# Kernel tuning notes

Measured on AMD Instinct MI355X. Metric: run time of the kernel, lower is better.

The kernel has to match this reference:

```python
import jax, jax.numpy as jnp
import numpy as np


def setup_inputs() -> dict:
    key = jax.random.key(0)
    ks = jax.random.split(key, 5)
    B, C, L, A = 32, 512, 8192, 128
    x = jax.random.normal(ks[0], (B, C, L), dtype=jnp.float32)
    Wq = jax.random.normal(ks[1], (A, C), dtype=jnp.float32) * 0.02
    Wk = jax.random.normal(ks[2], (A, C), dtype=jnp.float32) * 0.02
    Wv = jax.random.normal(ks[3], (A, C), dtype=jnp.float32) * 0.02
    Wout = jax.random.normal(ks[4], (C, A), dtype=jnp.float32) * 0.02
    return {"x": x, "Wq": Wq, "Wk": Wk, "Wv": Wv, "Wout": Wout, "center_idx": 4096}


def reference(x, Wq, Wk, Wv, Wout, center_idx):
    # x: [B, C, L]; W*: [attn_dim, C] (torch Linear weight layout); Wout: [C, attn_dim]
    A = Wq.shape[0]
    xc = x[:, :, center_idx]                      # [B, C] center feature
    q = xc @ Wq.T                                 # [B, A]
    xt = jnp.swapaxes(x, 1, 2)                    # [B, L, C]
    k = jnp.einsum('blc,ac->bla', xt, Wk)         # [B, L, A]
    v = jnp.einsum('blc,ac->bla', xt, Wv)         # [B, L, A]
    attn = jnp.einsum('bla,ba->bl', k, q) / jnp.sqrt(jnp.asarray(A, x.dtype))
    w = jax.nn.softmax(attn, axis=-1)             # [B, L]
    pooled = jnp.einsum('bla,bl->ba', v, w)       # [B, A]
    pooled = pooled @ Wout.T                      # [B, C]
    return (pooled, w)
```

## Files before the change

### kernel.cpp

```cpp
#include <hip/hip_runtime.h>
#include <math.h>

#define B_ 32
#define C_ 512
#define L_ 8192
#define A_ 128

__global__ __launch_bounds__(128) void k1_qk(const float* __restrict__ x,
                                             const float* __restrict__ Wq,
                                             const float* __restrict__ Wk,
                                             const int* __restrict__ cidx,
                                             float* __restrict__ qk) {
  __shared__ float xc[C_];
  __shared__ float q[A_];
  const int b = blockIdx.x, tid = threadIdx.x;
  const int ci = cidx[0];
  const float* xb = x + (size_t)b * C_ * L_;
  for (int c = tid; c < C_; c += 128) xc[c] = xb[(size_t)c * L_ + ci];
  __syncthreads();
  {
    float acc = 0.f;
    const float* wq = Wq + tid * C_;
    for (int c = 0; c < C_; ++c) acc += xc[c] * wq[c];
    q[tid] = acc;
  }
  __syncthreads();
  const float scale = 0.08838834764831845f;
  for (int c = tid; c < C_; c += 128) {
    float s = 0.f;
    for (int a = 0; a < A_; ++a) s += q[a] * Wk[a * C_ + c];
    qk[b * C_ + c] = s * scale;
  }
}

__global__ __launch_bounds__(128) void k2_attn(const float* __restrict__ x,
                                               const float* __restrict__ qk,
                                               float* __restrict__ attn) {
  __shared__ float qks[C_];
  const int b = blockIdx.y, tid = threadIdx.x;
  const int l = blockIdx.x * 512 + tid * 4;
  for (int c = tid; c < C_; c += 128) qks[c] = qk[b * C_ + c];
  __syncthreads();
  const float* xb = x + (size_t)b * C_ * L_ + l;
  float4 acc = make_float4(0.f, 0.f, 0.f, 0.f);
#pragma unroll 8
  for (int c = 0; c < C_; ++c) {
    const float4 xv4 = *reinterpret_cast<const float4*>(xb + (size_t)c * L_);
    const float s = qks[c];
    acc.x += s * xv4.x;
    acc.y += s * xv4.y;
    acc.z += s * xv4.z;
    acc.w += s * xv4.w;
  }
  *reinterpret_cast<float4*>(attn + b * L_ + l) = acc;
}

__global__ __launch_bounds__(256) void k3_softmax(const float* __restrict__ attn,
                                                  float* __restrict__ w) {
  const int b = blockIdx.x, tid = threadIdx.x;
  const float* ab = attn + b * L_;
  float4 vals[8];
  float m = -INFINITY;
#pragma unroll
  for (int i = 0; i < 8; ++i) {
    vals[i] = *reinterpret_cast<const float4*>(ab + (size_t)(i * 256 + tid) * 4);
    m = fmaxf(m, fmaxf(fmaxf(vals[i].x, vals[i].y), fmaxf(vals[i].z, vals[i].w)));
  }
  __shared__ float sm[256];
  sm[tid] = m;
  __syncthreads();
  for (int s = 128; s > 0; s >>= 1) {
    if (tid < s) sm[tid] = fmaxf(sm[tid], sm[tid + s]);
    __syncthreads();
  }
  m = sm[0];
  __syncthreads();
  float sum = 0.f;
#pragma unroll
  for (int i = 0; i < 8; ++i) {
    vals[i].x = __expf(vals[i].x - m);
    vals[i].y = __expf(vals[i].y - m);
    vals[i].z = __expf(vals[i].z - m);
    vals[i].w = __expf(vals[i].w - m);
    sum += vals[i].x + vals[i].y + vals[i].z + vals[i].w;
  }
  sm[tid] = sum;
  __syncthreads();
  for (int s = 128; s > 0; s >>= 1) {
    if (tid < s) sm[tid] += sm[tid + s];
    __syncthreads();
  }
  const float inv = 1.f / sm[0];
  float* wb = w + b * L_;
#pragma unroll
  for (int i = 0; i < 8; ++i) {
    float4 o;
    o.x = vals[i].x * inv;
    o.y = vals[i].y * inv;
    o.z = vals[i].z * inv;
    o.w = vals[i].w * inv;
    *reinterpret_cast<float4*>(wb + (size_t)(i * 256 + tid) * 4) = o;
  }
}

__global__ __launch_bounds__(256) void k4_xv(const float* __restrict__ x,
                                             const float* __restrict__ w,
                                             float* __restrict__ xv) {
  const int b = blockIdx.y, c = blockIdx.x, tid = threadIdx.x;
  const float* row = x + ((size_t)b * C_ + c) * L_;
  const float* wb = w + b * L_;
  float acc = 0.f;
#pragma unroll
  for (int i = 0; i < 8; ++i) {
    const int l = (i * 256 + tid) * 4;
    const float4 xr = *reinterpret_cast<const float4*>(row + l);
    const float4 wr = *reinterpret_cast<const float4*>(wb + l);
    acc += xr.x * wr.x + xr.y * wr.y + xr.z * wr.z + xr.w * wr.w;
  }
  __shared__ float sm[256];
  sm[tid] = acc;
  __syncthreads();
  for (int s = 128; s > 0; s >>= 1) {
    if (tid < s) sm[tid] += sm[tid + s];
    __syncthreads();
  }
  if (tid == 0) xv[b * C_ + c] = sm[0];
}

__global__ __launch_bounds__(128) void k5_out(const float* __restrict__ xv,
                                              const float* __restrict__ Wv,
                                              const float* __restrict__ Wout,
                                              float* __restrict__ out) {
  __shared__ float xvs[C_];
  __shared__ float pv[A_];
  const int b = blockIdx.x, tid = threadIdx.x;
  for (int c = tid; c < C_; c += 128) xvs[c] = xv[b * C_ + c];
  __syncthreads();
  {
    float acc = 0.f;
    const float* wv = Wv + tid * C_;
    for (int c = 0; c < C_; ++c) acc += xvs[c] * wv[c];
    pv[tid] = acc;
  }
  __syncthreads();
  for (int co = tid; co < C_; co += 128) {
    float acc = 0.f;
    const float* wo = Wout + co * A_;
    for (int a = 0; a < A_; ++a) acc += pv[a] * wo[a];
    out[b * C_ + co] = acc;
  }
}

extern "C" void kernel_launch(void* const* d_in, const int* in_sizes, int n_in,
                              void* d_out, int out_size, void* d_ws, size_t ws_size,
                              hipStream_t stream) {
  const float* x = (const float*)d_in[0];
  const float* Wq = (const float*)d_in[1];
  const float* Wk = (const float*)d_in[2];
  const float* Wv = (const float*)d_in[3];
  const float* Wout = (const float*)d_in[4];
  const int* cidx = (const int*)d_in[5];

  float* out_pooled = (float*)d_out;
  float* out_w = out_pooled + B_ * C_;

  float* qk = (float*)d_ws;
  float* attn = qk + B_ * C_;
  float* xv = attn + (size_t)B_ * L_;

  k1_qk<<<B_, 128, 0, stream>>>(x, Wq, Wk, cidx, qk);
  k2_attn<<<dim3(L_ / 512, B_), 128, 0, stream>>>(x, qk, attn);
  k3_softmax<<<B_, 256, 0, stream>>>(attn, out_w);
  k4_xv<<<dim3(C_, B_), 256, 0, stream>>>(x, out_w, xv);
  k5_out<<<B_, 128, 0, stream>>>(xv, Wv, Wout, out_pooled);
}
```

Baseline: 813.4 us.

## Fuse attention scores, local softmax and x·w pooling into one pass over x

Each block now loads a 512x32 tile of x into shared memory once. From that tile it computes the attention logits, a tile-local max and exp-sum, and partial weighted sums of x with the unnormalised probabilities. Small combine kernels then rescale the partials with the global max and normaliser, flash-attention style. This removes the second full read of the 537 MB x tensor. The cost is a larger workspace for per-tile partials (B*256*C floats), plus reading attn again to produce w.

Measured after the change: 790.1 us. 2.9% less time.

```diff
diff --git a/kernel.cpp b/kernel.cpp
--- a/kernel.cpp
+++ b/kernel.cpp
@@ -5,6 +5,8 @@
 #define C_ 512
 #define L_ 8192
 #define A_ 128
+#define LT_ 32
+#define NBLK_ (L_ / LT_)
 
 __global__ __launch_bounds__(128) void k1_qk(const float* __restrict__ x,
                                              const float* __restrict__ Wq,
@@ -33,98 +35,129 @@
   }
 }
 
-__global__ __launch_bounds__(128) void k2_attn(const float* __restrict__ x,
-                                               const float* __restrict__ qk,
-                                               float* __restrict__ attn) {
+__global__ __launch_bounds__(256) void kf_fused(const float* __restrict__ x,
+                                                const float* __restrict__ qk,
+                                                float* __restrict__ attn,
+                                                float* __restrict__ mpart,
+                                                float* __restrict__ zpart,
+                                                float* __restrict__ xvp) {
+  __shared__ float xs[C_][LT_ + 1];
   __shared__ float qks[C_];
-  const int b = blockIdx.y, tid = threadIdx.x;
-  const int l = blockIdx.x * 512 + tid * 4;
-  for (int c = tid; c < C_; c += 128) qks[c] = qk[b * C_ + c];
-  __syncthreads();
-  const float* xb = x + (size_t)b * C_ * L_ + l;
-  float4 acc = make_float4(0.f, 0.f, 0.f, 0.f);
+  __shared__ float p[LT_];
+  __shared__ float red[8][LT_];
+  const int tid = threadIdx.x;
+  const int blk = blockIdx.x;
+  const int b = blockIdx.y;
+  const int l0 = blk * LT_;
+  const float* xb = x + (size_t)b * C_ * L_;
+
+  qks[tid] = qk[b * C_ + tid];
+  qks[tid + 256] = qk[b * C_ + tid + 256];
+#pragma unroll
+  for (int i = 0; i < 16; ++i) {
+    const int idx = i * 256 + tid;
+    const int c = idx >> 3;
+    const int li = (idx & 7) * 4;
+    const float4 v = *reinterpret_cast<const float4*>(xb + (size_t)c * L_ + l0 + li);
+    xs[c][li] = v.x; xs[c][li + 1] = v.y; xs[c][li + 2] = v.z; xs[c][li + 3] = v.w;
+  }
+  __syncthreads();
+
+  const int l = tid & 31, g = tid >> 5;
+  {
+    float part = 0.f;
+    const int cbase = g * 64;
 #pragma unroll 8
-  for (int c = 0; c < C_; ++c) {
-    const float4 xv4 = *reinterpret_cast<const float4*>(xb + (size_t)c * L_);
-    const float s = qks[c];
-    acc.x += s * xv4.x;
-    acc.y += s * xv4.y;
-    acc.z += s * xv4.z;
-    acc.w += s * xv4.w;
-  }
-  *reinterpret_cast<float4*>(attn + b * L_ + l) = acc;
-}
-
-__global__ __launch_bounds__(256) void k3_softmax(const float* __restrict__ attn,
-                                                  float* __restrict__ w) {
+    for (int c = cbase; c < cbase + 64; ++c) part += qks[c] * xs[c][l];
+    red[g][l] = part;
+  }
+  __syncthreads();
+  if (tid < 32) {
+    float a = 0.f;
+#pragma unroll
+    for (int gg = 0; gg < 8; ++gg) a += red[gg][l];
+    attn[b * L_ + l0 + l] = a;
+    float m = a;
+#pragma unroll
+    for (int o = 16; o > 0; o >>= 1) m = fmaxf(m, __shfl_xor(m, o, 32));
+    const float pv = __expf(a - m);
+    float z = pv;
+#pragma unroll
+    for (int o = 16; o > 0; o >>= 1) z += __shfl_xor(z, o, 32);
+    p[l] = pv;
+    if (l == 0) { mpart[b * NBLK_ + blk] = m; zpart[b * NBLK_ + blk] = z; }
+  }
+  __syncthreads();
+
+#pragma unroll
+  for (int k = 0; k < 2; ++k) {
+    const int c = tid + k * 256;
+    float acc = 0.f;
+#pragma unroll
+    for (int ll = 0; ll < LT_; ++ll) acc += p[ll] * xs[c][ll];
+    xvp[((size_t)b * NBLK_ + blk) * C_ + c] = acc;
+  }
+}
+
+__global__ __launch_bounds__(256) void kc1(const float* __restrict__ mpart,
+                                           const float* __restrict__ zpart,
+                                           const float* __restrict__ attn,
+                                           float* __restrict__ sc,
+                                           float* __restrict__ minvz,
+                                           float* __restrict__ w) {
   const int b = blockIdx.x, tid = threadIdx.x;
-  const float* ab = attn + b * L_;
-  float4 vals[8];
-  float m = -INFINITY;
-#pragma unroll
-  for (int i = 0; i < 8; ++i) {
-    vals[i] = *reinterpret_cast<const float4*>(ab + (size_t)(i * 256 + tid) * 4);
-    m = fmaxf(m, fmaxf(fmaxf(vals[i].x, vals[i].y), fmaxf(vals[i].z, vals[i].w)));
-  }
   __shared__ float sm[256];
+  const float m = mpart[b * NBLK_ + tid];
   sm[tid] = m;
   __syncthreads();
   for (int s = 128; s > 0; s >>= 1) {
     if (tid < s) sm[tid] = fmaxf(sm[tid], sm[tid + s]);
     __syncthreads();
   }
-  m = sm[0];
-  __syncthreads();
-  float sum = 0.f;
-#pragma unroll
-  for (int i = 0; i < 8; ++i) {
-    vals[i].x = __expf(vals[i].x - m);
-    vals[i].y = __expf(vals[i].y - m);
-    vals[i].z = __expf(vals[i].z - m);
-    vals[i].w = __expf(vals[i].w - m);
-    sum += vals[i].x + vals[i].y + vals[i].z + vals[i].w;
-  }
-  sm[tid] = sum;
+  const float M = sm[0];
+  __syncthreads();
+  const float e = __expf(m - M);
+  sm[tid] = e * zpart[b * NBLK_ + tid];
   __syncthreads();
   for (int s = 128; s > 0; s >>= 1) {
     if (tid < s) sm[tid] += sm[tid + s];
     __syncthreads();
   }
-  const float inv = 1.f / sm[0];
+  const float invZ = 1.f / sm[0];
+  sc[b * NBLK_ + tid] = e;
+  if (tid == 0) { minvz[b * 2] = M; minvz[b * 2 + 1] = invZ; }
+  const float* ab = attn + b * L_;
   float* wb = w + b * L_;
 #pragma unroll
   for (int i = 0; i < 8; ++i) {
-    float4 o;
-    o.x = vals[i].x * inv;
-    o.y = vals[i].y * inv;
-    o.z = vals[i].z * inv;
-    o.w = vals[i].w * inv;
-    *reinterpret_cast<float4*>(wb + (size_t)(i * 256 + tid) * 4) = o;
-  }
-}
-
-__global__ __launch_bounds__(256) void k4_xv(const float* __restrict__ x,
-                                             const float* __restrict__ w,
-                                             float* __restrict__ xv) {
-  const int b = blockIdx.y, c = blockIdx.x, tid = threadIdx.x;
-  const float* row = x + ((size_t)b * C_ + c) * L_;
-  const float* wb = w + b * L_;
+    const int li = (i * 256 + tid) * 4;
+    float4 v = *reinterpret_cast<const float4*>(ab + li);
+    v.x = __expf(v.x - M) * invZ;
+    v.y = __expf(v.y - M) * invZ;
+    v.z = __expf(v.z - M) * invZ;
+    v.w = __expf(v.w - M) * invZ;
+    *reinterpret_cast<float4*>(wb + li) = v;
+  }
+}
+
+__global__ __launch_bounds__(256) void kc2(const float* __restrict__ xvp,
+                                           const float* __restrict__ sc,
+                                           const float* __restrict__ minvz,
+                                           float* __restrict__ xv) {
+  const int b = blockIdx.y, cg = blockIdx.x, tid = threadIdx.x;
+  const int cl = tid & 63, bs = tid >> 6;
+  __shared__ float red[4][64];
+  const float* base = xvp + (size_t)b * NBLK_ * C_ + cg * 64 + cl;
+  const float* scb = sc + b * NBLK_;
   float acc = 0.f;
-#pragma unroll
-  for (int i = 0; i < 8; ++i) {
-    const int l = (i * 256 + tid) * 4;
-    const float4 xr = *reinterpret_cast<const float4*>(row + l);
-    const float4 wr = *reinterpret_cast<const float4*>(wb + l);
-    acc += xr.x * wr.x + xr.y * wr.y + xr.z * wr.z + xr.w * wr.w;
-  }
-  __shared__ float sm[256];
-  sm[tid] = acc;
-  __syncthreads();
-  for (int s = 128; s > 0; s >>= 1) {
-    if (tid < s) sm[tid] += sm[tid + s];
-    __syncthreads();
-  }
-  if (tid == 0) xv[b * C_ + c] = sm[0];
+  for (int blk = bs * 64; blk < bs * 64 + 64; ++blk)
+    acc += scb[blk] * base[(size_t)blk * C_];
+  red[bs][cl] = acc;
+  __syncthreads();
+  if (tid < 64) {
+    const float v = red[0][tid] + red[1][tid] + red[2][tid] + red[3][tid];
+    xv[b * C_ + cg * 64 + tid] = v * minvz[b * 2 + 1];
+  }
 }
 
 __global__ __launch_bounds__(128) void k5_out(const float* __restrict__ xv,
@@ -164,13 +197,19 @@
   float* out_pooled = (float*)d_out;
   float* out_w = out_pooled + B_ * C_;
 
-  float* qk = (float*)d_ws;
-  float* attn = qk + B_ * C_;
-  float* xv = attn + (size_t)B_ * L_;
+  float* p = (float*)d_ws;
+  float* qk = p;        p += B_ * C_;
+  float* attn = p;      p += (size_t)B_ * L_;
+  float* mpart = p;     p += B_ * NBLK_;
+  float* zpart = p;     p += B_ * NBLK_;
+  float* sc = p;        p += B_ * NBLK_;
+  float* minvz = p;     p += B_ * 2;
+  float* xvp = p;       p += (size_t)B_ * NBLK_ * C_;
+  float* xv = p;        p += B_ * C_;
 
   k1_qk<<<B_, 128, 0, stream>>>(x, Wq, Wk, cidx, qk);
-  k2_attn<<<dim3(L_ / 512, B_), 128, 0, stream>>>(x, qk, attn);
-  k3_softmax<<<B_, 256, 0, stream>>>(attn, out_w);
-  k4_xv<<<dim3(C_, B_), 256, 0, stream>>>(x, out_w, xv);
+  kf_fused<<<dim3(NBLK_, B_), 256, 0, stream>>>(x, qk, attn, mpart, zpart, xvp);
+  kc1<<<B_, 256, 0, stream>>>(mpart, zpart, attn, sc, minvz, out_w);
+  kc2<<<dim3(8, B_), 256, 0, stream>>>(xvp, sc, minvz, xv);
   k5_out<<<B_, 128, 0, stream>>>(xv, Wv, Wout, out_pooled);
 }
```
